# Kernel optimization log

Hardware: AMD Instinct MI355X
Metric: run time of the kernel (lower is better)

The kernel has to match this reference:

```python
import jax, jax.numpy as jnp
import numpy as np

N = 50000
EPS = 1e-5


def _layernorm(x, g, b):
    mu = jnp.mean(x, axis=-1, keepdims=True)
    var = jnp.mean((x - mu) ** 2, axis=-1, keepdims=True)
    return (x - mu) * jax.lax.rsqrt(var + EPS) * g + b


def _gcn_conv(x, W, b, src, dst, norm, n):
    # PyG GCNConv: x' = D^{-1/2}(A+I)D^{-1/2} (x W) + b, self-loops already in src/dst
    xw = x @ W                                   # [N, F_out]
    msg = xw[src] * norm[:, None]                # gather + scale, [E+N, F_out]
    return jax.ops.segment_sum(msg, dst, num_segments=n) + b


def _prep_edges(edge_index, n):
    loops = jnp.arange(n, dtype=edge_index.dtype)
    src = jnp.concatenate([edge_index[0], loops])
    dst = jnp.concatenate([edge_index[1], loops])
    deg = jax.ops.segment_sum(jnp.ones(dst.shape[0], jnp.float32), dst, num_segments=n)
    dinv = jnp.where(deg > 0, jax.lax.rsqrt(deg), 0.0)
    norm = dinv[src] * dinv[dst]
    return src, dst, norm


def setup_inputs() -> dict:
    key = jax.random.key(0)
    ks = jax.random.split(key, 8)
    gene, hid, nc = 512, 256, 4
    x = jax.random.normal(ks[0], (N, gene), jnp.float32)
    edge_index = jax.random.randint(ks[1], (2, 1600000), 0, N, dtype=jnp.int64)

    def lin(k, fi, fo):
        return jax.random.normal(k, (fi, fo), jnp.float32) / np.sqrt(fi)

    d = {
        "x": x, "edge_index": edge_index,
        "W1": lin(ks[2], gene, hid), "b1": jnp.zeros(hid, jnp.float32),
        "W2": lin(ks[3], hid, 2 * hid), "b2": jnp.zeros(2 * hid, jnp.float32),
        "W3": lin(ks[4], 2 * hid, hid), "b3": jnp.zeros(hid, jnp.float32),
        "W4": lin(ks[5], hid, hid // 2), "b4": jnp.zeros(hid // 2, jnp.float32),
        "Wc": lin(ks[6], hid // 2, nc), "bc": jnp.zeros(nc, jnp.float32),
        "g1": jnp.ones(hid, jnp.float32), "be1": jnp.zeros(hid, jnp.float32),
        "g2": jnp.ones(2 * hid, jnp.float32), "be2": jnp.zeros(2 * hid, jnp.float32),
        "g3": jnp.ones(hid, jnp.float32), "be3": jnp.zeros(hid, jnp.float32),
        "g4": jnp.ones(hid // 2, jnp.float32), "be4": jnp.zeros(hid // 2, jnp.float32),
    }
    return d


def reference(x, edge_index, W1, b1, W2, b2, W3, b3, W4, b4, Wc, bc,
              g1, be1, g2, be2, g3, be3, g4, be4):
    n = x.shape[0]
    src, dst, norm = _prep_edges(edge_index, n)
    # dropout layers are identity (training=False)
    h1 = jax.nn.elu(_layernorm(_gcn_conv(x, W1, b1, src, dst, norm, n), g1, be1))
    h2 = jax.nn.elu(_layernorm(_gcn_conv(h1, W2, b2, src, dst, norm, n), g2, be2))
    h3 = jax.nn.elu(_layernorm(_gcn_conv(h2, W3, b3, src, dst, norm, n), g3, be3))
    h4_in = h3 + h1
    out_conv = _gcn_conv(h4_in, W4, b4, src, dst, norm, n)
    out_bn = _layernorm(out_conv, g4, be4)
    h = jax.nn.elu(out_bn)
    return (h @ Wc + bc, out_conv, out_bn)
```

## Files before the change

kernel.cpp:

```cpp
#include <hip/hip_runtime.h>
#include <hip/hip_bf16.h>
#include <math.h>

typedef unsigned short u16;
typedef u16 us8 __attribute__((ext_vector_type(8)));
typedef u16 us4 __attribute__((ext_vector_type(4)));
typedef float f32x4 __attribute__((ext_vector_type(4)));
typedef float f32x8 __attribute__((ext_vector_type(8)));
typedef __bf16 bf8 __attribute__((ext_vector_type(8)));

#define SCAN_B 256
#define CH 8192

__device__ __forceinline__ float bf2f(u16 v) {
    unsigned u = ((unsigned)v) << 16;
    return __builtin_bit_cast(float, u);
}
__device__ __forceinline__ u16 f2bf(float f) {
    unsigned u = __builtin_bit_cast(unsigned, f);
    unsigned lsb = (u >> 16) & 1;
    u += 0x7fff + lsb;
    return (u16)(u >> 16);
}
__device__ __forceinline__ void fma8(f32x8& acc, float w, us8 v) {
#pragma unroll
    for (int j = 0; j < 8; j++) acc[j] += w * bf2f(v[j]);
}

__global__ void detect_k(const int* __restrict__ ei, int E,
                         const u16* __restrict__ xraw, int* flag) {
    __shared__ int c_i32, c_f32;
    if (threadIdx.x == 0) { c_i32 = 0; c_f32 = 0; }
    __syncthreads();
    int ne = (E < 4096) ? E : 4096;
    for (int e = threadIdx.x; e < ne; e += blockDim.x)
        if (ei[2 * e + 1] != 0) c_i32 = 1;
    for (int k = threadIdx.x; k < 8192; k += blockDim.x) {
        u16 v = xraw[2 * k];
        int ex = (v >> 7) & 0xFF;
        if (ex >= 0xF0) atomicAdd(&c_f32, 1);
    }
    __syncthreads();
    if (threadIdx.x == 0) {
        flag[0] = (c_i32 == 0) ? 1 : 0;
        flag[1] = (c_f32 >= 4) ? 1 : 0;
    }
}

__global__ void cvt_x_k(const void* __restrict__ src, u16* __restrict__ dst,
                        long nq, const int* __restrict__ flag) {
    int f32m = flag[1];
    long i0 = (long)blockIdx.x * blockDim.x + threadIdx.x;
    long stride = (long)gridDim.x * blockDim.x;
    if (f32m) {
        const f32x4* s = (const f32x4*)src;
        for (long i = i0; i < nq; i += stride) {
            f32x4 v = s[i];
            us4 o;
            #pragma unroll
            for (int j = 0; j < 4; j++) o[j] = f2bf(v[j]);
            ((us4*)dst)[i] = o;
        }
    } else {
        const us4* s = (const us4*)src;
        for (long i = i0; i < nq; i += stride) ((us4*)dst)[i] = s[i];
    }
}

__global__ void cvt_wt_k(const void* __restrict__ W, u16* __restrict__ Wt,
                         int K, int Nn, const int* __restrict__ flag) {
    int t = blockIdx.x * blockDim.x + threadIdx.x;
    if (t >= K * Nn) return;
    int k = t / Nn, nn = t - k * Nn;
    u16 b;
    if (flag[1]) b = f2bf(((const float*)W)[t]);
    else         b = ((const u16*)W)[t];
    Wt[nn * K + k] = b;
}

struct PEnt { const void* s; int n; int off; };
struct PTab { PEnt e[14]; };
__global__ void cvt_params_k(PTab tab, float* __restrict__ pbuf,
                             const int* __restrict__ flag) {
    PEnt en = tab.e[blockIdx.x];
    int f32m = flag[1];
    for (int i = threadIdx.x; i < en.n; i += blockDim.x) {
        float v = f32m ? ((const float*)en.s)[i] : bf2f(((const u16*)en.s)[i]);
        pbuf[en.off + i] = v;
    }
}

__global__ void init_counts_k(int* counts, int n) {
    int i = blockIdx.x * blockDim.x + threadIdx.x;
    if (i < n) counts[i] = 1;
}

__global__ void histA_k(const int* __restrict__ ei, const int* __restrict__ flag,
                        int* __restrict__ hist, int E, int n, int NB, int NBUK, int shiftv) {
    __shared__ int lh[256];
    int blk = blockIdx.x;
    for (int b = threadIdx.x; b < NBUK; b += 256) lh[b] = 0;
    __syncthreads();
    int e0 = blk * CH;
    int e1 = min(e0 + CH, E);
    int i64 = flag[0];
    for (int e = e0 + threadIdx.x; e < e1; e += 256) {
        int d;
        if (i64) d = (int)((const long long*)ei)[(size_t)E + e];
        else     d = ei[(size_t)E + e];
        int b = ((unsigned)d < (unsigned)n) ? min(d >> shiftv, NBUK - 1) : (NBUK - 1);
        atomicAdd(&lh[b], 1);
    }
    __syncthreads();
    for (int b = threadIdx.x; b < NBUK; b += 256) hist[b * NB + blk] = lh[b];
}

__global__ void scan1_k(const int* __restrict__ counts, int* incl, int* bsum, int n) {
    __shared__ int tmp[SCAN_B];
    int t = threadIdx.x;
    int i = blockIdx.x * SCAN_B + t;
    int v = (i < n) ? counts[i] : 0;
    tmp[t] = v;
    __syncthreads();
    for (int o = 1; o < SCAN_B; o <<= 1) {
        int x = 0;
        if (t >= o) x = tmp[t - o];
        __syncthreads();
        if (t >= o) tmp[t] += x;
        __syncthreads();
    }
    if (i < n) incl[i] = tmp[t];
    if (t == SCAN_B - 1) bsum[blockIdx.x] = tmp[t];
}

__global__ void scan2_k(const int* __restrict__ bsum, int* bscan, int nb) {
    __shared__ int tmp[SCAN_B];
    int t = threadIdx.x;
    tmp[t] = (t < nb) ? bsum[t] : 0;
    __syncthreads();
    for (int o = 1; o < SCAN_B; o <<= 1) {
        int x = 0;
        if (t >= o) x = tmp[t - o];
        __syncthreads();
        if (t >= o) tmp[t] += x;
        __syncthreads();
    }
    bscan[t] = tmp[t];
}

__global__ void exclA_k(const int* __restrict__ incl, const int* __restrict__ bscan,
                        const int* __restrict__ hist, int* __restrict__ ofs, int len) {
    int i = blockIdx.x * 256 + threadIdx.x;
    if (i < len) {
        int boff = (blockIdx.x > 0) ? bscan[blockIdx.x - 1] : 0;
        ofs[i] = incl[i] + boff - hist[i];
    }
}

__global__ void scatC_k(const int* __restrict__ ei, const int* __restrict__ flag,
                        const int* __restrict__ ofs, long long* __restrict__ ebuf,
                        int E, int n, int NB, int NBUK, int shiftv) {
    __shared__ int cur[256];
    int blk = blockIdx.x;
    for (int b = threadIdx.x; b < NBUK; b += 256) cur[b] = ofs[b * NB + blk];
    __syncthreads();
    int e0 = blk * CH;
    int e1 = min(e0 + CH, E);
    int i64 = flag[0];
    for (int e = e0 + threadIdx.x; e < e1; e += 256) {
        int s, d;
        if (i64) {
            const long long* e64 = (const long long*)ei;
            s = (int)e64[e]; d = (int)e64[(size_t)E + e];
        } else {
            s = ei[e]; d = ei[(size_t)E + e];
        }
        int b = ((unsigned)d < (unsigned)n) ? min(d >> shiftv, NBUK - 1) : (NBUK - 1);
        int pos = atomicAdd(&cur[b], 1);
        ebuf[pos] = ((long long)(unsigned)d << 32) | (unsigned)s;
    }
}

__global__ void count_ebuf_k(const long long* __restrict__ ebuf, int* counts, int E, int n) {
    int e = blockIdx.x * blockDim.x + threadIdx.x;
    if (e >= E) return;
    long long pr = ebuf[e];
    int d = (int)(pr >> 32);
    if ((unsigned)d < (unsigned)n) atomicAdd(&counts[d], 1);
}

__global__ void dinv_k(const int* __restrict__ counts, float* dinv, int n) {
    int i = blockIdx.x * blockDim.x + threadIdx.x;
    if (i < n) dinv[i] = rsqrtf((float)counts[i]);
}

__global__ void rowptr_k(const int* __restrict__ incl, const int* __restrict__ bscan,
                         int* rowptr, int n) {
    int i = blockIdx.x * blockDim.x + threadIdx.x;
    if (i < n) {
        int boff = (blockIdx.x > 0) ? bscan[blockIdx.x - 1] : 0;
        rowptr[i + 1] = incl[i] + boff;
        if (i == 0) rowptr[0] = 0;
    }
}

__global__ void cursor_k(const int* __restrict__ rowptr, int* cursor, int n) {
    int i = blockIdx.x * blockDim.x + threadIdx.x;
    if (i < n) cursor[i] = rowptr[i];
}

__global__ void scatD_k(const long long* __restrict__ ebuf, int* cursor,
                        int* __restrict__ col, int E, int n) {
    int e = blockIdx.x * blockDim.x + threadIdx.x;
    if (e < E) {
        long long pr = ebuf[e];
        int d = (int)(pr >> 32);
        int s = (int)(pr & 0xffffffffLL);
        if ((unsigned)s < (unsigned)n && (unsigned)d < (unsigned)n) {
            int pos = atomicAdd(&cursor[d], 1);
            col[pos] = s;
        }
    } else if (e < E + n) {
        int i = e - E;
        int pos = atomicAdd(&cursor[i], 1);
        col[pos] = i;
    }
}

typedef __attribute__((address_space(1))) const void gas_v;
typedef __attribute__((address_space(3))) void las_v;

__global__ __launch_bounds__(256) void gemm128_k(
    const u16* __restrict__ A, const u16* __restrict__ Bt,
    u16* __restrict__ C, int M, int K, int Nn) {
    __shared__ u16 As[128 * 32];
    __shared__ u16 Bs[128 * 32];
    int tid = threadIdx.x;
    int wave = tid >> 6;
    int lane = tid & 63;
    int wr = (wave >> 1) * 64;
    int wc = (wave & 1) * 64;
    long row0 = (long)blockIdx.x * 128;
    int col0 = blockIdx.y * 128;
    int lr = lane >> 2;
    int lc = lane & 3;
    int m = lane & 15;
    int q = lane >> 4;

    f32x4 acc[4][4];
    #pragma unroll
    for (int i = 0; i < 4; i++)
        #pragma unroll
        for (int j = 0; j < 4; j++) acc[i][j] = (f32x4){0.f, 0.f, 0.f, 0.f};

    for (int k0 = 0; k0 < K; k0 += 32) {
        #pragma unroll
        for (int p = 0; p < 2; p++) {
            int c = wave + p * 4;
            long ar = row0 + c * 16 + lr;
            if (ar > (long)M - 1) ar = (long)M - 1;
            const u16* ga = A + ar * K + k0 + lc * 8;
            __builtin_amdgcn_global_load_lds((gas_v*)ga, (las_v*)&As[c * 512], 16, 0, 0);
            int br = col0 + c * 16 + lr;
            const u16* gb = Bt + (size_t)br * K + k0 + lc * 8;
            __builtin_amdgcn_global_load_lds((gas_v*)gb, (las_v*)&Bs[c * 512], 16, 0, 0);
        }
        __syncthreads();

        us8 av[4], bv[4];
        #pragma unroll
        for (int i = 0; i < 4; i++) {
            av[i] = *(const us8*)&As[(wr + i * 16 + m) * 32 + q * 8];
            bv[i] = *(const us8*)&Bs[(wc + i * 16 + m) * 32 + q * 8];
        }
        #pragma unroll
        for (int i = 0; i < 4; i++) {
            bf8 fa = __builtin_bit_cast(bf8, av[i]);
            #pragma unroll
            for (int j = 0; j < 4; j++) {
                bf8 fb = __builtin_bit_cast(bf8, bv[j]);
                acc[i][j] = __builtin_amdgcn_mfma_f32_16x16x32_bf16(fa, fb, acc[i][j], 0, 0, 0);
            }
        }
        __syncthreads();
    }

    #pragma unroll
    for (int i = 0; i < 4; i++) {
        #pragma unroll
        for (int r = 0; r < 4; r++) {
            long row = row0 + wr + i * 16 + q * 4 + r;
            if (row < M) {
                #pragma unroll
                for (int j = 0; j < 4; j++)
                    C[row * Nn + col0 + wc + j * 16 + m] = f2bf(acc[i][j][r]);
            }
        }
    }
}

__global__ __launch_bounds__(256) void agg_k(
    const u16* __restrict__ in, const int* __restrict__ rowptr,
    const int* __restrict__ col, const float* __restrict__ dinv,
    const float* __restrict__ bias, const float* __restrict__ gamma,
    const float* __restrict__ beta, u16* __restrict__ out_h,
    const u16* __restrict__ resid, void* __restrict__ final_base,
    const int* __restrict__ flag, const float* __restrict__ Wcf,
    const float* __restrict__ bcf, int F, int nN) {
    int wv = threadIdx.x >> 6;
    int lane = threadIdx.x & 63;
    int i = blockIdx.x * 4 + wv;
    if (i >= nN) return;

    int rowt = F >> 3;
    int Gw = 64 / rowt;
    int g = lane / rowt;
    int f0 = (lane & (rowt - 1)) << 3;

    int beg = rowptr[i], end = rowptr[i + 1];
    f32x8 acc = {0, 0, 0, 0, 0, 0, 0, 0}, acc2 = acc, acc3 = acc, acc4 = acc;
    int e = beg + g;
    for (; e + 3 * Gw < end; e += 4 * Gw) {
        int s0 = col[e], s1 = col[e + Gw], s2 = col[e + 2 * Gw], s3 = col[e + 3 * Gw];
        s0 = ((unsigned)s0 < (unsigned)nN) ? s0 : 0;
        s1 = ((unsigned)s1 < (unsigned)nN) ? s1 : 0;
        s2 = ((unsigned)s2 < (unsigned)nN) ? s2 : 0;
        s3 = ((unsigned)s3 < (unsigned)nN) ? s3 : 0;
        float w0 = dinv[s0], w1 = dinv[s1], w2 = dinv[s2], w3 = dinv[s3];
        us8 v0 = *(const us8*)(in + (unsigned)(s0 * F) + f0);
        us8 v1 = *(const us8*)(in + (unsigned)(s1 * F) + f0);
        us8 v2 = *(const us8*)(in + (unsigned)(s2 * F) + f0);
        us8 v3 = *(const us8*)(in + (unsigned)(s3 * F) + f0);
        fma8(acc, w0, v0);
        fma8(acc2, w1, v1);
        fma8(acc3, w2, v2);
        fma8(acc4, w3, v3);
    }
    for (; e + Gw < end; e += 2 * Gw) {
        int s0 = col[e], s1 = col[e + Gw];
        s0 = ((unsigned)s0 < (unsigned)nN) ? s0 : 0;
        s1 = ((unsigned)s1 < (unsigned)nN) ? s1 : 0;
        float w0 = dinv[s0], w1 = dinv[s1];
        us8 v0 = *(const us8*)(in + (unsigned)(s0 * F) + f0);
        us8 v1 = *(const us8*)(in + (unsigned)(s1 * F) + f0);
        fma8(acc, w0, v0);
        fma8(acc2, w1, v1);
    }
    if (e < end) {
        int s = col[e];
        s = ((unsigned)s < (unsigned)nN) ? s : 0;
        us8 v = *(const us8*)(in + (unsigned)(s * F) + f0);
        fma8(acc, dinv[s], v);
    }
    #pragma unroll
    for (int j = 0; j < 8; j++) acc[j] = (acc[j] + acc2[j]) + (acc3[j] + acc4[j]);

    for (int o = 32; o >= rowt; o >>= 1) {
        #pragma unroll
        for (int j = 0; j < 8; j++) acc[j] += __shfl_down(acc[j], o);
    }
    bool active = lane < rowt;
    float di = dinv[i];

    if (!bias) {
        if (active) {
            us8 o8;
            #pragma unroll
            for (int j = 0; j < 8; j++) o8[j] = f2bf(di * acc[j]);
            *(us8*)(out_h + (unsigned)(i * F) + f0) = o8;
        }
        return;
    }

    f32x8 accv = {0, 0, 0, 0, 0, 0, 0, 0};
    if (active) {
        #pragma unroll
        for (int j = 0; j < 8; j++) accv[j] = di * acc[j] + bias[f0 + j];
    }
    int f32m = final_base ? flag[1] : 0;
    if (final_base && active) {
        size_t conv_idx = (size_t)nN * 4 + (size_t)i * F + f0;
        if (f32m) {
            #pragma unroll
            for (int j = 0; j < 8; j++) ((float*)final_base)[conv_idx + j] = accv[j];
        } else {
            us8 o8;
            #pragma unroll
            for (int j = 0; j < 8; j++) o8[j] = f2bf(accv[j]);
            *(us8*)((u16*)final_base + conv_idx) = o8;
        }
    }

    float p1 = 0.f, p2 = 0.f;
    #pragma unroll
    for (int j = 0; j < 8; j++) { p1 += accv[j]; p2 += accv[j] * accv[j]; }
    for (int o = rowt >> 1; o >= 1; o >>= 1) {
        p1 += __shfl_xor(p1, o);
        p2 += __shfl_xor(p2, o);
    }
    float invF = 1.0f / (float)F;
    float mu = p1 * invF;
    float var = fmaxf(p2 * invF - mu * mu, 0.f);
    float rstd = rsqrtf(var + 1e-5f);

    f32x8 h8 = {0, 0, 0, 0, 0, 0, 0, 0};
    if (active) {
        f32x8 y8;
        #pragma unroll
        for (int j = 0; j < 8; j++)
            y8[j] = (accv[j] - mu) * rstd * gamma[f0 + j] + beta[f0 + j];
        if (final_base) {
            size_t bn_idx = (size_t)nN * 4 + (size_t)nN * F + (size_t)i * F + f0;
            if (f32m) {
                #pragma unroll
                for (int j = 0; j < 8; j++) ((float*)final_base)[bn_idx + j] = y8[j];
            } else {
                us8 o8;
                #pragma unroll
                for (int j = 0; j < 8; j++) o8[j] = f2bf(y8[j]);
                *(us8*)((u16*)final_base + bn_idx) = o8;
            }
        }
        #pragma unroll
        for (int j = 0; j < 8; j++) h8[j] = (y8[j] > 0.f) ? y8[j] : expm1f(y8[j]);
        if (resid) {
            us8 r8 = *(const us8*)(resid + (unsigned)(i * F) + f0);
            #pragma unroll
            for (int j = 0; j < 8; j++) h8[j] += bf2f(r8[j]);
        }
        if (out_h) {
            us8 o8;
            #pragma unroll
            for (int j = 0; j < 8; j++) o8[j] = f2bf(h8[j]);
            *(us8*)(out_h + (unsigned)(i * F) + f0) = o8;
        }
    }

    if (Wcf) {
        float s0 = 0.f, s1 = 0.f, s2 = 0.f, s3 = 0.f;
        if (active) {
            #pragma unroll
            for (int j = 0; j < 8; j++) {
                const float* wr = Wcf + (f0 + j) * 4;
                s0 += h8[j] * wr[0];
                s1 += h8[j] * wr[1];
                s2 += h8[j] * wr[2];
                s3 += h8[j] * wr[3];
            }
        }
        for (int o = rowt >> 1; o >= 1; o >>= 1) {
            s0 += __shfl_xor(s0, o);
            s1 += __shfl_xor(s1, o);
            s2 += __shfl_xor(s2, o);
            s3 += __shfl_xor(s3, o);
        }
        if (lane == 0) {
            size_t lidx = (size_t)i * 4;
            if (f32m) {
                ((float*)final_base)[lidx + 0] = s0 + bcf[0];
                ((float*)final_base)[lidx + 1] = s1 + bcf[1];
                ((float*)final_base)[lidx + 2] = s2 + bcf[2];
                ((float*)final_base)[lidx + 3] = s3 + bcf[3];
            } else {
                ((u16*)final_base)[lidx + 0] = f2bf(s0 + bcf[0]);
                ((u16*)final_base)[lidx + 1] = f2bf(s1 + bcf[1]);
                ((u16*)final_base)[lidx + 2] = f2bf(s2 + bcf[2]);
                ((u16*)final_base)[lidx + 3] = f2bf(s3 + bcf[3]);
            }
        }
    }
}

__global__ __launch_bounds__(256) void ln_elu_k(u16* __restrict__ h,
                                                const float* __restrict__ bias,
                                                const float* __restrict__ gamma,
                                                const float* __restrict__ beta, int nN) {
    int wv = threadIdx.x >> 6;
    int lane = threadIdx.x & 63;
    int i = blockIdx.x * 4 + wv;
    if (i >= nN) return;
    int f0 = lane * 8;
    size_t base = (size_t)i * 512 + f0;
    us8 v8 = *(const us8*)(h + base);
    f32x8 v;
    #pragma unroll
    for (int j = 0; j < 8; j++) v[j] = bf2f(v8[j]) + bias[f0 + j];
    float p1 = 0.f, p2 = 0.f;
    #pragma unroll
    for (int j = 0; j < 8; j++) { p1 += v[j]; p2 += v[j] * v[j]; }
    #pragma unroll
    for (int o = 32; o >= 1; o >>= 1) {
        p1 += __shfl_xor(p1, o);
        p2 += __shfl_xor(p2, o);
    }
    const float invF = 1.0f / 512.0f;
    float mu = p1 * invF;
    float var = fmaxf(p2 * invF - mu * mu, 0.f);
    float rstd = rsqrtf(var + 1e-5f);
    us8 o8;
    #pragma unroll
    for (int j = 0; j < 8; j++) {
        float y = (v[j] - mu) * rstd * gamma[f0 + j] + beta[f0 + j];
        y = (y > 0.f) ? y : expm1f(y);
        o8[j] = f2bf(y);
    }
    *(us8*)(h + base) = o8;
}

__global__ void marker_k(float* out) {
    if (threadIdx.x == 0 && blockIdx.x == 0) {
        out[0] = 31337.0f; out[1] = 31337.0f;
    }
}

extern "C" void kernel_launch(void* const* d_in, const int* in_sizes, int n_in,
                              void* d_out, int out_size, void* d_ws, size_t ws_size,
                              hipStream_t stream) {
    const int N = in_sizes[0] / 512;
    const int E = in_sizes[1] / 2;

    const void* x  = d_in[0];
    const int* ei  = (const int*)d_in[1];

    char* p = (char*)d_ws;
    auto alloc = [&](size_t bytes) -> void* {
        void* r = (void*)p;
        p += (bytes + 255) & ~(size_t)255;
        return r;
    };
    int*   flag   = (int*)alloc(256);
    int*   counts = (int*)alloc((size_t)N * 4);
    int*   rowptr = (int*)alloc((size_t)(N + 1) * 4);
    int*   cursor = (int*)alloc((size_t)N * 4);
    int*   incl   = (int*)alloc((size_t)N * 4);
    int*   bsum   = (int*)alloc(256 * 4);
    int*   bscan  = (int*)alloc(256 * 4);
    float* dinv   = (float*)alloc((size_t)N * 4);
    int*   col    = (int*)alloc((size_t)(E + N) * 4);
    float* pbuf   = (float*)alloc(4096 * 4);
    u16* W1t = (u16*)alloc((size_t)512 * 256 * 2);
    u16* W2t = (u16*)alloc((size_t)256 * 512 * 2);
    u16* W3t = (u16*)alloc((size_t)512 * 256 * 2);
    u16* W4t = (u16*)alloc((size_t)256 * 128 * 2);
    u16* bigA = (u16*)alloc((size_t)N * 512 * 2);
    u16* xw   = (u16*)alloc((size_t)N * 256 * 2);
    u16* h1   = (u16*)alloc((size_t)N * 256 * 2);

    size_t needed = (size_t)(p - (char*)d_ws);
    if (needed > ws_size) {
        marker_k<<<1, 64, 0, stream>>>((float*)d_out);
        return;
    }

    u16* xbf = bigA;
    u16* h2  = bigA;

    int shiftv = 8;
    while (((N - 1) >> shiftv) > 255) shiftv++;
    int NBUK = ((N - 1) >> shiftv) + 1;
    int NB_E = (E + CH - 1) / CH;
    int flatlen = NBUK * NB_E;
    int NH = (flatlen + 255) / 256;
    long long* ebuf = (long long*)xw;
    int* hist     = (int*)h1;
    int* histincl = hist + flatlen;
    int* ofs      = histincl + flatlen;

    PTab tab;
    tab.e[0]  = { d_in[3],  256, 0    };
    tab.e[1]  = { d_in[12], 256, 256  };
    tab.e[2]  = { d_in[13], 256, 512  };
    tab.e[3]  = { d_in[5],  512, 768  };
    tab.e[4]  = { d_in[14], 512, 1280 };
    tab.e[5]  = { d_in[15], 512, 1792 };
    tab.e[6]  = { d_in[7],  256, 2304 };
    tab.e[7]  = { d_in[16], 256, 2560 };
    tab.e[8]  = { d_in[17], 256, 2816 };
    tab.e[9]  = { d_in[9],  128, 3072 };
    tab.e[10] = { d_in[18], 128, 3200 };
    tab.e[11] = { d_in[19], 128, 3328 };
    tab.e[12] = { d_in[10], 512, 3456 };
    tab.e[13] = { d_in[11], 4,   3968 };
    float* b1f = pbuf + 0,   *g1f = pbuf + 256,  *be1f = pbuf + 512;
    float* b2f = pbuf + 768, *g2f = pbuf + 1280, *be2f = pbuf + 1792;
    float* b3f = pbuf + 2304,*g3f = pbuf + 2560, *be3f = pbuf + 2816;
    float* b4f = pbuf + 3072,*g4f = pbuf + 3200, *be4f = pbuf + 3328;
    float* Wcf = pbuf + 3456,*bcf = pbuf + 3968;

    int nb1 = (N + 255) / 256;
    int NB = (N + SCAN_B - 1) / SCAN_B;

    detect_k<<<1, 256, 0, stream>>>(ei, E, (const u16*)x, flag);

    cvt_x_k<<<4096, 256, 0, stream>>>(x, xbf, (long)N * 512 / 4, flag);
    cvt_wt_k<<<(512 * 256 + 255) / 256, 256, 0, stream>>>(d_in[2], W1t, 512, 256, flag);
    cvt_wt_k<<<(256 * 512 + 255) / 256, 256, 0, stream>>>(d_in[4], W2t, 256, 512, flag);
    cvt_wt_k<<<(512 * 256 + 255) / 256, 256, 0, stream>>>(d_in[6], W3t, 512, 256, flag);
    cvt_wt_k<<<(256 * 128 + 255) / 256, 256, 0, stream>>>(d_in[8], W4t, 256, 128, flag);
    cvt_params_k<<<14, 256, 0, stream>>>(tab, pbuf, flag);

    histA_k<<<NB_E, 256, 0, stream>>>(ei, flag, hist, E, N, NB_E, NBUK, shiftv);
    scan1_k<<<NH, SCAN_B, 0, stream>>>(hist, histincl, bsum, flatlen);
    scan2_k<<<1, SCAN_B, 0, stream>>>(bsum, bscan, NH);
    exclA_k<<<NH, 256, 0, stream>>>(histincl, bscan, hist, ofs, flatlen);
    scatC_k<<<NB_E, 256, 0, stream>>>(ei, flag, ofs, ebuf, E, N, NB_E, NBUK, shiftv);
    init_counts_k<<<nb1, 256, 0, stream>>>(counts, N);
    count_ebuf_k<<<(E + 255) / 256, 256, 0, stream>>>(ebuf, counts, E, N);
    dinv_k<<<nb1, 256, 0, stream>>>(counts, dinv, N);
    scan1_k<<<NB, SCAN_B, 0, stream>>>(counts, incl, bsum, N);
    scan2_k<<<1, SCAN_B, 0, stream>>>(bsum, bscan, NB);
    rowptr_k<<<NB, SCAN_B, 0, stream>>>(incl, bscan, rowptr, N);
    cursor_k<<<nb1, 256, 0, stream>>>(rowptr, cursor, N);
    scatD_k<<<(E + N + 255) / 256, 256, 0, stream>>>(ebuf, cursor, col, E, N);

    int gx = (N + 127) / 128;
    int ga = (N + 3) / 4;

    gemm128_k<<<dim3(gx, 256 / 128), 256, 0, stream>>>(xbf, W1t, xw, N, 512, 256);
    agg_k<<<ga, 256, 0, stream>>>(xw, rowptr, col, dinv, b1f, g1f, be1f,
                                  h1, nullptr, nullptr, flag, nullptr, nullptr, 256, N);
    agg_k<<<ga, 256, 0, stream>>>(h1, rowptr, col, dinv, nullptr, nullptr, nullptr,
                                  xw, nullptr, nullptr, flag, nullptr, nullptr, 256, N);
    gemm128_k<<<dim3(gx, 512 / 128), 256, 0, stream>>>(xw, W2t, h2, N, 256, 512);
    ln_elu_k<<<ga, 256, 0, stream>>>(h2, b2f, g2f, be2f, N);
    gemm128_k<<<dim3(gx, 256 / 128), 256, 0, stream>>>(h2, W3t, xw, N, 512, 256);
    agg_k<<<ga, 256, 0, stream>>>(xw, rowptr, col, dinv, b3f, g3f, be3f,
                                  h1, h1, nullptr, flag, nullptr, nullptr, 256, N);
    gemm128_k<<<dim3(gx, 128 / 128), 256, 0, stream>>>(h1, W4t, xw, N, 256, 128);
    agg_k<<<ga, 256, 0, stream>>>(xw, rowptr, col, dinv, b4f, g4f, be4f,
                                  nullptr, nullptr, d_out, flag, Wcf, bcf, 128, N);
}
```

Measured before the change: 1.003 ms.

## Merge preprocessing kernels, remap GEMM block order, shrink aggregation unroll

The four weight-transpose launches become one, degree counting moves into the scatter kernel, and rowptr, cursor and dinv are computed in a single finalize kernel. This removes several launches and one extra pass over the edge buffer. The GEMM uses a 1D grid with a grouped block order so that 8 row tiles share column tiles and L2 reuse improves. The aggregation loop loses its 4-way unrolled path and keeps only the 2-way one, which lowers register use but exposes less memory-level parallelism per wave.

Result: no change. 984.3 us (-1.8%).

```diff
diff --git a/kernel.cpp b/kernel.cpp
--- a/kernel.cpp
+++ b/kernel.cpp
@@ -67,15 +67,18 @@
     }
 }
 
-__global__ void cvt_wt_k(const void* __restrict__ W, u16* __restrict__ Wt,
-                         int K, int Nn, const int* __restrict__ flag) {
+struct WEnt { const void* s; u16* dst; int K; int Nn; int base; };
+__global__ void cvt_wts_k(WEnt e0, WEnt e1, WEnt e2, WEnt e3,
+                          const int* __restrict__ flag, int total) {
     int t = blockIdx.x * blockDim.x + threadIdx.x;
-    if (t >= K * Nn) return;
-    int k = t / Nn, nn = t - k * Nn;
+    if (t >= total) return;
+    WEnt en = (t >= e3.base) ? e3 : ((t >= e2.base) ? e2 : ((t >= e1.base) ? e1 : e0));
+    int li = t - en.base;
+    int k = li / en.Nn, nn = li - k * en.Nn;
     u16 b;
-    if (flag[1]) b = f2bf(((const float*)W)[t]);
-    else         b = ((const u16*)W)[t];
-    Wt[nn * K + k] = b;
+    if (flag[1]) b = f2bf(((const float*)en.s)[li]);
+    else         b = ((const u16*)en.s)[li];
+    en.dst[nn * en.K + k] = b;
 }
 
 struct PEnt { const void* s; int n; int off; };
@@ -159,6 +162,7 @@
 
 __global__ void scatC_k(const int* __restrict__ ei, const int* __restrict__ flag,
                         const int* __restrict__ ofs, long long* __restrict__ ebuf,
+                        int* __restrict__ counts,
                         int E, int n, int NB, int NBUK, int shiftv) {
     __shared__ int cur[256];
     int blk = blockIdx.x;
@@ -178,35 +182,22 @@
         int b = ((unsigned)d < (unsigned)n) ? min(d >> shiftv, NBUK - 1) : (NBUK - 1);
         int pos = atomicAdd(&cur[b], 1);
         ebuf[pos] = ((long long)(unsigned)d << 32) | (unsigned)s;
-    }
-}
-
-__global__ void count_ebuf_k(const long long* __restrict__ ebuf, int* counts, int E, int n) {
-    int e = blockIdx.x * blockDim.x + threadIdx.x;
-    if (e >= E) return;
-    long long pr = ebuf[e];
-    int d = (int)(pr >> 32);
-    if ((unsigned)d < (unsigned)n) atomicAdd(&counts[d], 1);
-}
-
-__global__ void dinv_k(const int* __restrict__ counts, float* dinv, int n) {
-    int i = blockIdx.x * blockDim.x + threadIdx.x;
-    if (i < n) dinv[i] = rsqrtf((float)counts[i]);
-}
-
-__global__ void rowptr_k(const int* __restrict__ incl, const int* __restrict__ bscan,
-                         int* rowptr, int n) {
-    int i = blockIdx.x * blockDim.x + threadIdx.x;
+        if ((unsigned)d < (unsigned)n) atomicAdd(&counts[d], 1);
+    }
+}
+
+__global__ void finCSR_k(const int* __restrict__ incl, const int* __restrict__ bscan,
+                         const int* __restrict__ counts, int* __restrict__ rowptr,
+                         int* __restrict__ cursor, float* __restrict__ dinv, int n) {
+    int i = blockIdx.x * SCAN_B + threadIdx.x;
     if (i < n) {
         int boff = (blockIdx.x > 0) ? bscan[blockIdx.x - 1] : 0;
-        rowptr[i + 1] = incl[i] + boff;
+        int rp_end = incl[i] + boff;
+        rowptr[i + 1] = rp_end;
         if (i == 0) rowptr[0] = 0;
-    }
-}
-
-__global__ void cursor_k(const int* __restrict__ rowptr, int* cursor, int n) {
-    int i = blockIdx.x * blockDim.x + threadIdx.x;
-    if (i < n) cursor[i] = rowptr[i];
+        cursor[i] = rp_end - counts[i];
+        dinv[i] = rsqrtf((float)counts[i]);
+    }
 }
 
 __global__ void scatD_k(const long long* __restrict__ ebuf, int* cursor,
@@ -232,7 +223,23 @@
 
 __global__ __launch_bounds__(256) void gemm128_k(
     const u16* __restrict__ A, const u16* __restrict__ Bt,
-    u16* __restrict__ C, int M, int K, int Nn) {
+    u16* __restrict__ C, int M, int K, int Nn, int nyv) {
+    int nx = (M + 127) >> 7;
+    int nfull = nx & ~7;
+    int cutoff = nfull * nyv;
+    int b = blockIdx.x;
+    int bx, by;
+    if (b < cutoff) {
+        int k = b & 7;
+        int q = b >> 3;
+        by = q % nyv;
+        bx = (q / nyv) * 8 + k;
+    } else {
+        int r = b - cutoff;
+        bx = nfull + r / nyv;
+        by = r % nyv;
+    }
+
     __shared__ u16 As[128 * 32];
     __shared__ u16 Bs[128 * 32];
     int tid = threadIdx.x;
@@ -240,8 +247,8 @@
     int lane = tid & 63;
     int wr = (wave >> 1) * 64;
     int wc = (wave & 1) * 64;
-    long row0 = (long)blockIdx.x * 128;
-    int col0 = blockIdx.y * 128;
+    long row0 = (long)bx * 128;
+    int col0 = by * 128;
     int lr = lane >> 2;
     int lc = lane & 3;
     int m = lane & 15;
@@ -318,24 +325,8 @@
     int f0 = (lane & (rowt - 1)) << 3;
 
     int beg = rowptr[i], end = rowptr[i + 1];
-    f32x8 acc = {0, 0, 0, 0, 0, 0, 0, 0}, acc2 = acc, acc3 = acc, acc4 = acc;
+    f32x8 acc = {0, 0, 0, 0, 0, 0, 0, 0}, acc2 = acc;
     int e = beg + g;
-    for (; e + 3 * Gw < end; e += 4 * Gw) {
-        int s0 = col[e], s1 = col[e + Gw], s2 = col[e + 2 * Gw], s3 = col[e + 3 * Gw];
-        s0 = ((unsigned)s0 < (unsigned)nN) ? s0 : 0;
-        s1 = ((unsigned)s1 < (unsigned)nN) ? s1 : 0;
-        s2 = ((unsigned)s2 < (unsigned)nN) ? s2 : 0;
-        s3 = ((unsigned)s3 < (unsigned)nN) ? s3 : 0;
-        float w0 = dinv[s0], w1 = dinv[s1], w2 = dinv[s2], w3 = dinv[s3];
-        us8 v0 = *(const us8*)(in + (unsigned)(s0 * F) + f0);
-        us8 v1 = *(const us8*)(in + (unsigned)(s1 * F) + f0);
-        us8 v2 = *(const us8*)(in + (unsigned)(s2 * F) + f0);
-        us8 v3 = *(const us8*)(in + (unsigned)(s3 * F) + f0);
-        fma8(acc, w0, v0);
-        fma8(acc2, w1, v1);
-        fma8(acc3, w2, v2);
-        fma8(acc4, w3, v3);
-    }
     for (; e + Gw < end; e += 2 * Gw) {
         int s0 = col[e], s1 = col[e + Gw];
         s0 = ((unsigned)s0 < (unsigned)nN) ? s0 : 0;
@@ -353,7 +344,7 @@
         fma8(acc, dinv[s], v);
     }
     #pragma unroll
-    for (int j = 0; j < 8; j++) acc[j] = (acc[j] + acc2[j]) + (acc3[j] + acc4[j]);
+    for (int j = 0; j < 8; j++) acc[j] += acc2[j];
 
     for (int o = 32; o >= rowt; o >>= 1) {
         #pragma unroll
@@ -593,40 +584,41 @@
     detect_k<<<1, 256, 0, stream>>>(ei, E, (const u16*)x, flag);
 
     cvt_x_k<<<4096, 256, 0, stream>>>(x, xbf, (long)N * 512 / 4, flag);
-    cvt_wt_k<<<(512 * 256 + 255) / 256, 256, 0, stream>>>(d_in[2], W1t, 512, 256, flag);
-    cvt_wt_k<<<(256 * 512 + 255) / 256, 256, 0, stream>>>(d_in[4], W2t, 256, 512, flag);
-    cvt_wt_k<<<(512 * 256 + 255) / 256, 256, 0, stream>>>(d_in[6], W3t, 512, 256, flag);
-    cvt_wt_k<<<(256 * 128 + 255) / 256, 256, 0, stream>>>(d_in[8], W4t, 256, 128, flag);
+    {
+        WEnt e0 = { d_in[2], W1t, 512, 256, 0 };
+        WEnt e1 = { d_in[4], W2t, 256, 512, 512 * 256 };
+        WEnt e2 = { d_in[6], W3t, 512, 256, 512 * 256 + 256 * 512 };
+        WEnt e3 = { d_in[8], W4t, 256, 128, 512 * 256 * 2 + 256 * 512 };
+        int total = 512 * 256 * 2 + 256 * 512 + 256 * 128;
+        cvt_wts_k<<<(total + 255) / 256, 256, 0, stream>>>(e0, e1, e2, e3, flag, total);
+    }
     cvt_params_k<<<14, 256, 0, stream>>>(tab, pbuf, flag);
 
+    init_counts_k<<<nb1, 256, 0, stream>>>(counts, N);
     histA_k<<<NB_E, 256, 0, stream>>>(ei, flag, hist, E, N, NB_E, NBUK, shiftv);
     scan1_k<<<NH, SCAN_B, 0, stream>>>(hist, histincl, bsum, flatlen);
     scan2_k<<<1, SCAN_B, 0, stream>>>(bsum, bscan, NH);
     exclA_k<<<NH, 256, 0, stream>>>(histincl, bscan, hist, ofs, flatlen);
-    scatC_k<<<NB_E, 256, 0, stream>>>(ei, flag, ofs, ebuf, E, N, NB_E, NBUK, shiftv);
-    init_counts_k<<<nb1, 256, 0, stream>>>(counts, N);
-    count_ebuf_k<<<(E + 255) / 256, 256, 0, stream>>>(ebuf, counts, E, N);
-    dinv_k<<<nb1, 256, 0, stream>>>(counts, dinv, N);
+    scatC_k<<<NB_E, 256, 0, stream>>>(ei, flag, ofs, ebuf, counts, E, N, NB_E, NBUK, shiftv);
     scan1_k<<<NB, SCAN_B, 0, stream>>>(counts, incl, bsum, N);
     scan2_k<<<1, SCAN_B, 0, stream>>>(bsum, bscan, NB);
-    rowptr_k<<<NB, SCAN_B, 0, stream>>>(incl, bscan, rowptr, N);
-    cursor_k<<<nb1, 256, 0, stream>>>(rowptr, cursor, N);
+    finCSR_k<<<NB, SCAN_B, 0, stream>>>(incl, bscan, counts, rowptr, cursor, dinv, N);
     scatD_k<<<(E + N + 255) / 256, 256, 0, stream>>>(ebuf, cursor, col, E, N);
 
     int gx = (N + 127) / 128;
     int ga = (N + 3) / 4;
 
-    gemm128_k<<<dim3(gx, 256 / 128), 256, 0, stream>>>(xbf, W1t, xw, N, 512, 256);
+    gemm128_k<<<gx * 2, 256, 0, stream>>>(xbf, W1t, xw, N, 512, 256, 2);
     agg_k<<<ga, 256, 0, stream>>>(xw, rowptr, col, dinv, b1f, g1f, be1f,
                                   h1, nullptr, nullptr, flag, nullptr, nullptr, 256, N);
     agg_k<<<ga, 256, 0, stream>>>(h1, rowptr, col, dinv, nullptr, nullptr, nullptr,
                                   xw, nullptr, nullptr, flag, nullptr, nullptr, 256, N);
-    gemm128_k<<<dim3(gx, 512 / 128), 256, 0, stream>>>(xw, W2t, h2, N, 256, 512);
+    gemm128_k<<<gx * 4, 256, 0, stream>>>(xw, W2t, h2, N, 256, 512, 4);
     ln_elu_k<<<ga, 256, 0, stream>>>(h2, b2f, g2f, be2f, N);
-    gemm128_k<<<dim3(gx, 256 / 128), 256, 0, stream>>>(h2, W3t, xw, N, 512, 256);
+    gemm128_k<<<gx * 2, 256, 0, stream>>>(h2, W3t, xw, N, 512, 256, 2);
     agg_k<<<ga, 256, 0, stream>>>(xw, rowptr, col, dinv, b3f, g3f, be3f,
                                   h1, h1, nullptr, flag, nullptr, nullptr, 256, N);
-    gemm128_k<<<dim3(gx, 128 / 128), 256, 0, stream>>>(h1, W4t, xw, N, 256, 128);
+    gemm128_k<<<gx * 1, 256, 0, stream>>>(h1, W4t, xw, N, 256, 128, 1);
     agg_k<<<ga, 256, 0, stream>>>(xw, rowptr, col, dinv, b4f, g4f, be4f,
                                   nullptr, nullptr, d_out, flag, Wcf, bcf, 128, N);
 }
```
